# Kernel tuning notes

Hardware: AMD Instinct MI355X
Metric: run time of the kernel (lower is better)

## Reference

```python
import jax, jax.numpy as jnp
import numpy as np

B, TQ, TY = 8, 400, 400
Q_DIM, Y_DIM, ATT_DIM = 256, 256, 128


def setup_inputs() -> dict:
    key = jax.random.key(0)
    ks = jax.random.split(key, 9)
    s_q = 1.0 / np.sqrt(Q_DIM)
    s_y = 1.0 / np.sqrt(Y_DIM)
    s_a = 1.0 / np.sqrt(ATT_DIM)
    return {
        "query": jax.random.normal(ks[0], (B, TQ, Q_DIM), jnp.float32),
        "y": jax.random.normal(ks[1], (B, TY, Y_DIM), jnp.float32),
        "Wq_w": jax.random.uniform(ks[2], (ATT_DIM, Q_DIM), jnp.float32, -s_q, s_q),
        "Wq_b": jax.random.uniform(ks[3], (ATT_DIM,), jnp.float32, -s_q, s_q),
        "Wy_w": jax.random.uniform(ks[4], (ATT_DIM, Y_DIM), jnp.float32, -s_y, s_y),
        "Wy_b": jax.random.uniform(ks[5], (ATT_DIM,), jnp.float32, -s_y, s_y),
        "v_w": jax.random.uniform(ks[6], (1, ATT_DIM), jnp.float32, -s_a, s_a),
        "v_b": jax.random.uniform(ks[7], (1,), jnp.float32, -s_a, s_a),
        "n_wins_y": jax.random.randint(ks[8], (B,), TY // 2, TY + 1, jnp.int64 if jax.config.jax_enable_x64 else jnp.int32),
    }


def reference(query, y, Wq_w, Wq_b, Wy_w, Wy_b, v_w, v_b, n_wins_y):
    # Bahdanau scores: tanh(Wq(q)[:,None,:,:] + Wy(y)[:,:,None,:]) -> [B,Ty,Tq,A]
    q_proj = jnp.einsum('bqd,ad->bqa', query, Wq_w) + Wq_b      # [B,Tq,A]
    y_proj = jnp.einsum('btd,ad->bta', y, Wy_w) + Wy_b          # [B,Ty,A]
    h = jnp.tanh(q_proj[:, None, :, :] + y_proj[:, :, None, :])  # [B,Ty,Tq,A]
    att = jnp.einsum('btqa,a->btq', h, v_w[0]) + v_b[0]          # [B,Ty,Tq]
    att = jnp.transpose(att, (0, 2, 1))                          # [B,Tq,Ty]
    # mask invalid y windows (dim 2 = Ty), then softmax over Ty
    mask = jnp.arange(att.shape[2])[None, None, :] < n_wins_y[:, None, None]
    att = jnp.where(mask, att, -jnp.inf)
    att = jax.nn.softmax(att, axis=2)
    # soft attention apply: bmm(att, y) -> [B,Tq,y_dim]
    return jnp.einsum('bqt,btd->bqd', att, y)
```

## Files before the change

kernel.cpp:

```cpp
#include <hip/hip_runtime.h>


#define LOG2E 1.4426950408889634f
#define TANH_SCALE 2.8853900817779268f

constexpr int TQn = 400, TYn = 400, AD = 128, DD = 256;

__global__ __launch_bounds__(128) void transpose_kernel(
    const float* __restrict__ Wq, const float* __restrict__ Wy,
    const float* __restrict__ vw,
    float4* __restrict__ WTq, float4* __restrict__ WTy,
    float* __restrict__ vneg)
{
    const int k4 = blockIdx.x & 63;
    const bool isq = blockIdx.x < 64;
    const float4* src = reinterpret_cast<const float4*>(isq ? Wq : Wy);
    float4* dst = isq ? WTq : WTy;
    const int a = threadIdx.x;
    dst[k4 * 128 + a] = src[a * 64 + k4];
    if (blockIdx.x == 0) vneg[a] = -2.f * vw[a];
}

__global__ __launch_bounds__(256, 4) void proj_kernel(
    const float* __restrict__ qin, const float* __restrict__ yin,
    const float4* __restrict__ WTq, const float* __restrict__ bq,
    const float4* __restrict__ WTy, const float* __restrict__ by,
    float* __restrict__ EqS, float* __restrict__ EyT)
{
    const int blk = blockIdx.x;
    const bool is_q = blk < 800;
    const int row0 = (is_q ? blk : blk - 800) * 4;
    const float* in   = (is_q ? qin : yin) + (size_t)row0 * DD;
    const float4* wt  = is_q ? WTq : WTy;
    const float* bias = is_q ? bq : by;

    __shared__ float lin[4 * DD];
    __shared__ float red[4][AD];
    {
        const float4* in4 = reinterpret_cast<const float4*>(in);
        reinterpret_cast<float4*>(lin)[threadIdx.x] = in4[threadIdx.x];
    }
    __syncthreads();

    const int a = threadIdx.x & 127;
    const int h = threadIdx.x >> 7;
    float acc[4] = {0.f, 0.f, 0.f, 0.f};
    const float4* l4 = reinterpret_cast<const float4*>(lin);
    #pragma unroll 8
    for (int i = 0; i < 32; ++i) {
        const int k4 = h * 32 + i;
        float4 w4 = wt[k4 * 128 + a];
        #pragma unroll
        for (int r = 0; r < 4; ++r) {
            float4 v = l4[r * 64 + k4];
            acc[r] = fmaf(w4.x, v.x, acc[r]);
            acc[r] = fmaf(w4.y, v.y, acc[r]);
            acc[r] = fmaf(w4.z, v.z, acc[r]);
            acc[r] = fmaf(w4.w, v.w, acc[r]);
        }
    }
    if (h) {
        #pragma unroll
        for (int r = 0; r < 4; ++r) red[r][a] = acc[r];
    }
    __syncthreads();
    if (!h) {
        const float bb = bias[a];
        const int a4 = a >> 2, ac = a & 3;
        const int qoff = (row0 & 7);
        #pragma unroll
        for (int r = 0; r < 4; ++r) {
            const float e = __builtin_amdgcn_exp2f(
                (acc[r] + red[r][a] + bb) * TANH_SCALE);
            if (is_q)
                EqS[(size_t)(row0 >> 3) * 1024 + a4 * 32 + (qoff + r) * 4 + ac] = e;
            else
                EyT[(size_t)a4 * 12800 + (size_t)(row0 + r) * 4 + ac] = e;
        }
    }
}

__global__ __launch_bounds__(448, 2) void score_kernel(
    const float* __restrict__ EqS,
    const float4* __restrict__ EyT4,
    const float* __restrict__ vneg,
    const int*  __restrict__ nwins,
    float* __restrict__ s)
{
    const int grp = blockIdx.x;
    const int b   = grp / 100;
    const int qg  = grp % 100;
    const int q0  = qg * 4;
    const int n   = nwins[b];
    const int t   = threadIdx.x;
    if ((t & ~63) >= n) return;

    const int ycol = b * TYn + min(t, TYn - 1);
    const float4* eqg = reinterpret_cast<const float4*>(EqS)
                      + (size_t)(b * 50 + (qg >> 1)) * 256 + 4 * (qg & 1);
    const float4* vn4 = reinterpret_cast<const float4*>(vneg);

    float ac0 = 0.f, ac1 = 0.f, ac2 = 0.f, ac3 = 0.f;
    for (int a4 = 0; a4 < 32; ++a4) {
        const float4 ey = EyT4[(size_t)a4 * 3200 + ycol];
        const float4* eqa = eqg + a4 * 8;
        const float4 vv = vn4[a4];
        const float4 e0 = eqa[0], e1 = eqa[1], e2 = eqa[2], e3 = eqa[3];
        #define SCORE_Q(ACC, EQ)                                            \
        {                                                                   \
            float a0 = fmaf(EQ.x, ey.x, 1.f);                               \
            float a1 = fmaf(EQ.y, ey.y, 1.f);                               \
            float a2 = fmaf(EQ.z, ey.z, 1.f);                               \
            float a3 = fmaf(EQ.w, ey.w, 1.f);                               \
            float p01 = a0 * a1, p23 = a2 * a3;                             \
            float R = __builtin_amdgcn_rcpf(p01 * p23);                     \
            float u = p23 * R, w = p01 * R;                                 \
            ACC = fmaf(vv.x, a1 * u, ACC);                                  \
            ACC = fmaf(vv.y, a0 * u, ACC);                                  \
            ACC = fmaf(vv.z, a3 * w, ACC);                                  \
            ACC = fmaf(vv.w, a2 * w, ACC);                                  \
        }
        SCORE_Q(ac0, e0) SCORE_Q(ac1, e1) SCORE_Q(ac2, e2) SCORE_Q(ac3, e3)
        #undef SCORE_Q
    }
    if (t < n) {
        float* srow = s + (size_t)(b * TQn + q0) * TYn + t;
        srow[0 * TYn] = ac0; srow[1 * TYn] = ac1;
        srow[2 * TYn] = ac2; srow[3 * TYn] = ac3;
    }
}

__global__ __launch_bounds__(256, 4) void apply_kernel(
    const float* __restrict__ y,
    const float* __restrict__ s,
    const int*  __restrict__ nwins,
    float* __restrict__ out)
{
    const int bid = blockIdx.x;
    const int b   = bid / 100;
    const int q0  = (bid % 100) * 4;
    const int tid = threadIdx.x, wave = tid >> 6, lane = tid & 63;
    const int n = nwins[b];
    const float NEG_INF = -__builtin_inff();

    __shared__ float  s_p[4][408];
    __shared__ float4 s_y[2][16 * 64];

    const float4* yb = reinterpret_cast<const float4*>(y) + (size_t)(b * TYn) * 64;
    const int scol = tid & 63, srow0 = tid >> 6;
    float4 g0 = yb[(size_t)(srow0     ) * 64 + scol];
    float4 g1 = yb[(size_t)(srow0 +  4) * 64 + scol];
    float4 g2 = yb[(size_t)(srow0 +  8) * 64 + scol];
    float4 g3 = yb[(size_t)(srow0 + 12) * 64 + scol];

    const float* srow = s + (size_t)(b * TQn + q0 + wave) * TYn;
    float sc0, sc1, sc2, sc3, sc4, sc5, sc6;
    {
        int t;
        t = 0 * 64 + lane; sc0 = (t < n) ? srow[t] : NEG_INF;
        t = 1 * 64 + lane; sc1 = (t < n) ? srow[t] : NEG_INF;
        t = 2 * 64 + lane; sc2 = (t < n) ? srow[t] : NEG_INF;
        t = 3 * 64 + lane; sc3 = (t < n) ? srow[t] : NEG_INF;
        t = 4 * 64 + lane; sc4 = (t < n) ? srow[t] : NEG_INF;
        t = 5 * 64 + lane; sc5 = (t < n) ? srow[t] : NEG_INF;
        t = 6 * 64 + lane; sc6 = (t < n) ? srow[t] : NEG_INF;
    }
    float m = fmaxf(fmaxf(fmaxf(sc0, sc1), fmaxf(sc2, sc3)),
                    fmaxf(fmaxf(sc4, sc5), sc6));
    #pragma unroll
    for (int off = 32; off >= 1; off >>= 1) m = fmaxf(m, __shfl_xor(m, off, 64));
    sc0 = __builtin_amdgcn_exp2f((sc0 - m) * LOG2E);
    sc1 = __builtin_amdgcn_exp2f((sc1 - m) * LOG2E);
    sc2 = __builtin_amdgcn_exp2f((sc2 - m) * LOG2E);
    sc3 = __builtin_amdgcn_exp2f((sc3 - m) * LOG2E);
    sc4 = __builtin_amdgcn_exp2f((sc4 - m) * LOG2E);
    sc5 = __builtin_amdgcn_exp2f((sc5 - m) * LOG2E);
    sc6 = __builtin_amdgcn_exp2f((sc6 - m) * LOG2E);
    float l = ((sc0 + sc1) + (sc2 + sc3)) + ((sc4 + sc5) + sc6);
    #pragma unroll
    for (int off = 32; off >= 1; off >>= 1) l += __shfl_xor(l, off, 64);
    const float inv = 1.0f / l;
    s_p[wave][0 * 64 + lane] = sc0 * inv;
    s_p[wave][1 * 64 + lane] = sc1 * inv;
    s_p[wave][2 * 64 + lane] = sc2 * inv;
    s_p[wave][3 * 64 + lane] = sc3 * inv;
    s_p[wave][4 * 64 + lane] = sc4 * inv;
    s_p[wave][5 * 64 + lane] = sc5 * inv;
    {
        const int t = 6 * 64 + lane;
        if (t < TYn) s_p[wave][t] = sc6 * inv;
    }

    const int q  = lane >> 4;
    const int d4 = (wave << 4) | (lane & 15);
    float4 acc = {0.f, 0.f, 0.f, 0.f};
    const int ntile = (n + 15) >> 4;

    __syncthreads();
    for (int i = 0; i < ntile; ++i) {
        float4* buf = s_y[i & 1];
        buf[(srow0     ) * 64 + scol] = g0;
        buf[(srow0 +  4) * 64 + scol] = g1;
        buf[(srow0 +  8) * 64 + scol] = g2;
        buf[(srow0 + 12) * 64 + scol] = g3;
        if (i + 1 < ntile) {
            const int t0n = (i + 1) * 16;
            g0 = yb[(size_t)(t0n + srow0     ) * 64 + scol];
            g1 = yb[(size_t)(t0n + srow0 +  4) * 64 + scol];
            g2 = yb[(size_t)(t0n + srow0 +  8) * 64 + scol];
            g3 = yb[(size_t)(t0n + srow0 + 12) * 64 + scol];
        }
        __syncthreads();
        const int tb = i * 16;
        #pragma unroll
        for (int ttl = 0; ttl < 16; ++ttl) {
            const float  pt = s_p[q][tb + ttl];
            const float4 yv = buf[ttl * 64 + d4];
            acc.x = fmaf(pt, yv.x, acc.x);
            acc.y = fmaf(pt, yv.y, acc.y);
            acc.z = fmaf(pt, yv.z, acc.z);
            acc.w = fmaf(pt, yv.w, acc.w);
        }
    }
    reinterpret_cast<float4*>(out)[(size_t)(b * TQn + q0 + q) * 64 + d4] = acc;
}

extern "C" void kernel_launch(void* const* d_in, const int* in_sizes, int n_in,
                              void* d_out, int out_size, void* d_ws, size_t ws_size,
                              hipStream_t stream) {
    const float* query = (const float*)d_in[0];
    const float* y     = (const float*)d_in[1];
    const float* Wq_w  = (const float*)d_in[2];
    const float* Wq_b  = (const float*)d_in[3];
    const float* Wy_w  = (const float*)d_in[4];
    const float* Wy_b  = (const float*)d_in[5];
    const float* v_w   = (const float*)d_in[6];
    const int* nw      = (const int*)d_in[8];
    float* out = (float*)d_out;

    float4* WTq  = (float4*)d_ws;
    float4* WTy  = WTq + 64 * 128;
    float*  vneg = (float*)(WTy + 64 * 128);
    float*  EqS  = vneg + 256;
    float*  EyT  = EqS + (size_t)400 * 1024;
    float*  s    = EyT + (size_t)32 * 3200 * 4;

    transpose_kernel<<<128, 128, 0, stream>>>(Wq_w, Wy_w, v_w, WTq, WTy, vneg);
    proj_kernel<<<1600, 256, 0, stream>>>(query, y, WTq, Wq_b, WTy, Wy_b, EqS, EyT);
    score_kernel<<<8 * 100, 448, 0, stream>>>(
        EqS, (const float4*)EyT, vneg, nw, s);
    apply_kernel<<<8 * 100, 256, 0, stream>>>(y, s, nw, out);
}
```

Baseline: 64.98 us.

## Restructure apply kernel to stream y from global into registers, 8 queries per block

The apply kernel now handles 8 queries per block with 512 threads instead of 4 queries with 256. It drops the double-buffered LDS staging of y tiles and its per-tile barriers. Each thread loads its y slice straight from global memory into a register double buffer and reads probabilities from LDS as float4. The loop always covers all 400 positions, relying on zero probabilities for masked positions rather than stopping at n. This removes LDS traffic and synchronisation but halves the block count, depends on the cache for y reuse, and adds work on the masked tail.

Result: slower. 91.08 us (+40.2%).

```diff
diff --git a/kernel.cpp b/kernel.cpp
--- a/kernel.cpp
+++ b/kernel.cpp
@@ -5,6 +5,7 @@
 #define TANH_SCALE 2.8853900817779268f
 
 constexpr int TQn = 400, TYn = 400, AD = 128, DD = 256;
+constexpr int PROW = 404;
 
 __global__ __launch_bounds__(128) void transpose_kernel(
     const float* __restrict__ Wq, const float* __restrict__ Wy,
@@ -130,28 +131,20 @@
     }
 }
 
-__global__ __launch_bounds__(256, 4) void apply_kernel(
+__global__ __launch_bounds__(512, 2) void apply_kernel(
     const float* __restrict__ y,
     const float* __restrict__ s,
     const int*  __restrict__ nwins,
     float* __restrict__ out)
 {
     const int bid = blockIdx.x;
-    const int b   = bid / 100;
-    const int q0  = (bid % 100) * 4;
+    const int b   = bid / 50;
+    const int q0  = (bid % 50) * 8;
     const int tid = threadIdx.x, wave = tid >> 6, lane = tid & 63;
     const int n = nwins[b];
     const float NEG_INF = -__builtin_inff();
 
-    __shared__ float  s_p[4][408];
-    __shared__ float4 s_y[2][16 * 64];
-
-    const float4* yb = reinterpret_cast<const float4*>(y) + (size_t)(b * TYn) * 64;
-    const int scol = tid & 63, srow0 = tid >> 6;
-    float4 g0 = yb[(size_t)(srow0     ) * 64 + scol];
-    float4 g1 = yb[(size_t)(srow0 +  4) * 64 + scol];
-    float4 g2 = yb[(size_t)(srow0 +  8) * 64 + scol];
-    float4 g3 = yb[(size_t)(srow0 + 12) * 64 + scol];
+    __shared__ __align__(16) float s_p[8][PROW];
 
     const float* srow = s + (size_t)(b * TQn + q0 + wave) * TYn;
     float sc0, sc1, sc2, sc3, sc4, sc5, sc6;
@@ -190,36 +183,48 @@
         const int t = 6 * 64 + lane;
         if (t < TYn) s_p[wave][t] = sc6 * inv;
     }
-
-    const int q  = lane >> 4;
-    const int d4 = (wave << 4) | (lane & 15);
+    __syncthreads();
+
+    const int q  = lane >> 3;
+    const int d4 = (wave << 3) | (lane & 7);
+    const float4* prow4 = reinterpret_cast<const float4*>(&s_p[q][0]);
+    const float4* yb4 = reinterpret_cast<const float4*>(y) + (size_t)(b * TYn) * 64;
     float4 acc = {0.f, 0.f, 0.f, 0.f};
-    const int ntile = (n + 15) >> 4;
-
-    __syncthreads();
-    for (int i = 0; i < ntile; ++i) {
-        float4* buf = s_y[i & 1];
-        buf[(srow0     ) * 64 + scol] = g0;
-        buf[(srow0 +  4) * 64 + scol] = g1;
-        buf[(srow0 +  8) * 64 + scol] = g2;
-        buf[(srow0 + 12) * 64 + scol] = g3;
-        if (i + 1 < ntile) {
-            const int t0n = (i + 1) * 16;
-            g0 = yb[(size_t)(t0n + srow0     ) * 64 + scol];
-            g1 = yb[(size_t)(t0n + srow0 +  4) * 64 + scol];
-            g2 = yb[(size_t)(t0n + srow0 +  8) * 64 + scol];
-            g3 = yb[(size_t)(t0n + srow0 + 12) * 64 + scol];
-        }
-        __syncthreads();
-        const int tb = i * 16;
-        #pragma unroll
-        for (int ttl = 0; ttl < 16; ++ttl) {
-            const float  pt = s_p[q][tb + ttl];
-            const float4 yv = buf[ttl * 64 + d4];
-            acc.x = fmaf(pt, yv.x, acc.x);
-            acc.y = fmaf(pt, yv.y, acc.y);
-            acc.z = fmaf(pt, yv.z, acc.z);
-            acc.w = fmaf(pt, yv.w, acc.w);
+
+    float4 a0 = yb4[      d4], a1 = yb4[ 64 + d4], a2 = yb4[128 + d4], a3 = yb4[192 + d4];
+    float4 b0 = yb4[256 + d4], b1 = yb4[320 + d4], b2 = yb4[384 + d4], b3 = yb4[448 + d4];
+
+    #pragma unroll 2
+    for (int t4 = 0; t4 < 100; t4 += 2) {
+        {
+            const float4 pv = prow4[t4];
+            acc.x = fmaf(pv.x, a0.x, acc.x); acc.y = fmaf(pv.x, a0.y, acc.y);
+            acc.z = fmaf(pv.x, a0.z, acc.z); acc.w = fmaf(pv.x, a0.w, acc.w);
+            acc.x = fmaf(pv.y, a1.x, acc.x); acc.y = fmaf(pv.y, a1.y, acc.y);
+            acc.z = fmaf(pv.y, a1.z, acc.z); acc.w = fmaf(pv.y, a1.w, acc.w);
+            acc.x = fmaf(pv.z, a2.x, acc.x); acc.y = fmaf(pv.z, a2.y, acc.y);
+            acc.z = fmaf(pv.z, a2.z, acc.z); acc.w = fmaf(pv.z, a2.w, acc.w);
+            acc.x = fmaf(pv.w, a3.x, acc.x); acc.y = fmaf(pv.w, a3.y, acc.y);
+            acc.z = fmaf(pv.w, a3.z, acc.z); acc.w = fmaf(pv.w, a3.w, acc.w);
+            if (t4 + 2 < 100) {
+                const float4* yr = yb4 + (size_t)(t4 + 2) * 256;
+                a0 = yr[d4]; a1 = yr[64 + d4]; a2 = yr[128 + d4]; a3 = yr[192 + d4];
+            }
+        }
+        {
+            const float4 pv = prow4[t4 + 1];
+            acc.x = fmaf(pv.x, b0.x, acc.x); acc.y = fmaf(pv.x, b0.y, acc.y);
+            acc.z = fmaf(pv.x, b0.z, acc.z); acc.w = fmaf(pv.x, b0.w, acc.w);
+            acc.x = fmaf(pv.y, b1.x, acc.x); acc.y = fmaf(pv.y, b1.y, acc.y);
+            acc.z = fmaf(pv.y, b1.z, acc.z); acc.w = fmaf(pv.y, b1.w, acc.w);
+            acc.x = fmaf(pv.z, b2.x, acc.x); acc.y = fmaf(pv.z, b2.y, acc.y);
+            acc.z = fmaf(pv.z, b2.z, acc.z); acc.w = fmaf(pv.z, b2.w, acc.w);
+            acc.x = fmaf(pv.w, b3.x, acc.x); acc.y = fmaf(pv.w, b3.y, acc.y);
+            acc.z = fmaf(pv.w, b3.z, acc.z); acc.w = fmaf(pv.w, b3.w, acc.w);
+            if (t4 + 3 < 100) {
+                const float4* yr = yb4 + (size_t)(t4 + 3) * 256;
+                b0 = yr[d4]; b1 = yr[64 + d4]; b2 = yr[128 + d4]; b3 = yr[192 + d4];
+            }
         }
     }
     reinterpret_cast<float4*>(out)[(size_t)(b * TQn + q0 + q) * 64 + d4] = acc;
@@ -249,5 +254,5 @@
     proj_kernel<<<1600, 256, 0, stream>>>(query, y, WTq, Wq_b, WTy, Wy_b, EqS, EyT);
     score_kernel<<<8 * 100, 448, 0, stream>>>(
         EqS, (const float4*)EyT, vneg, nw, s);
-    apply_kernel<<<8 * 100, 256, 0, stream>>>(y, s, nw, out);
-}
+    apply_kernel<<<8 * 50, 512, 0, stream>>>(y, s, nw, out);
+}
```

## Fuse score, softmax and attention-apply into one kernel

Applied to the files above, without the earlier changes.

Merges the score kernel and the apply kernel into a single kernel. Each block computes the 4x400 score tile, runs a block-wide softmax through LDS reductions, and multiplies the probabilities with y, with waves splitting the Ty rows and a final cross-wave reduction in LDS. This removes the global round-trip of the score matrix and one kernel launch. It also rewrites the score inner math to use a single combined numerator per reciprocal. The cost is that early-exit waves are no longer skipped: all 448 threads run the score loop and the apply loop over every row regardless of n, and extra syncs and LDS reductions are added.

After: 61.67 us. 5.1% less time.

```diff
diff --git a/kernel.cpp b/kernel.cpp
--- a/kernel.cpp
+++ b/kernel.cpp
@@ -80,22 +80,28 @@
     }
 }
 
-__global__ __launch_bounds__(448, 2) void score_kernel(
+__global__ __launch_bounds__(448, 2) void fused_kernel(
     const float* __restrict__ EqS,
     const float4* __restrict__ EyT4,
     const float* __restrict__ vneg,
+    const float* __restrict__ y,
     const int*  __restrict__ nwins,
-    float* __restrict__ s)
+    float* __restrict__ out)
 {
     const int grp = blockIdx.x;
     const int b   = grp / 100;
     const int qg  = grp % 100;
     const int q0  = qg * 4;
     const int n   = nwins[b];
-    const int t   = threadIdx.x;
-    if ((t & ~63) >= n) return;
-
-    const int ycol = b * TYn + min(t, TYn - 1);
+    const int tid = threadIdx.x;
+    const int wave = tid >> 6, lane = tid & 63;
+    const float NEG_INF = -__builtin_inff();
+
+    __shared__ __align__(16) float4 s_pT[448];
+    __shared__ __align__(16) float4 s_rbuf[7 * 128];
+    __shared__ float s_wred[2][7][4];
+
+    const int ycol = b * TYn + min(tid, TYn - 1);
     const float4* eqg = reinterpret_cast<const float4*>(EqS)
                       + (size_t)(b * 50 + (qg >> 1)) * 256 + 4 * (qg & 1);
     const float4* vn4 = reinterpret_cast<const float4*>(vneg);
@@ -112,117 +118,136 @@
             float a1 = fmaf(EQ.y, ey.y, 1.f);                               \
             float a2 = fmaf(EQ.z, ey.z, 1.f);                               \
             float a3 = fmaf(EQ.w, ey.w, 1.f);                               \
-            float p01 = a0 * a1, p23 = a2 * a3;                             \
-            float R = __builtin_amdgcn_rcpf(p01 * p23);                     \
-            float u = p23 * R, w = p01 * R;                                 \
-            ACC = fmaf(vv.x, a1 * u, ACC);                                  \
-            ACC = fmaf(vv.y, a0 * u, ACC);                                  \
-            ACC = fmaf(vv.z, a3 * w, ACC);                                  \
-            ACC = fmaf(vv.w, a2 * w, ACC);                                  \
+            float n01 = fmaf(vv.x, a1, vv.y * a0);                          \
+            float n23 = fmaf(vv.z, a3, vv.w * a2);                          \
+            float d01 = a0 * a1, d23 = a2 * a3;                             \
+            float N = fmaf(n01, d23, n23 * d01);                            \
+            float R = __builtin_amdgcn_rcpf(d01 * d23);                     \
+            ACC = fmaf(N, R, ACC);                                          \
         }
         SCORE_Q(ac0, e0) SCORE_Q(ac1, e1) SCORE_Q(ac2, e2) SCORE_Q(ac3, e3)
         #undef SCORE_Q
     }
-    if (t < n) {
-        float* srow = s + (size_t)(b * TQn + q0) * TYn + t;
-        srow[0 * TYn] = ac0; srow[1 * TYn] = ac1;
-        srow[2 * TYn] = ac2; srow[3 * TYn] = ac3;
-    }
-}
-
-__global__ __launch_bounds__(256, 4) void apply_kernel(
-    const float* __restrict__ y,
-    const float* __restrict__ s,
-    const int*  __restrict__ nwins,
-    float* __restrict__ out)
-{
-    const int bid = blockIdx.x;
-    const int b   = bid / 100;
-    const int q0  = (bid % 100) * 4;
-    const int tid = threadIdx.x, wave = tid >> 6, lane = tid & 63;
-    const int n = nwins[b];
-    const float NEG_INF = -__builtin_inff();
-
-    __shared__ float  s_p[4][408];
-    __shared__ float4 s_y[2][16 * 64];
-
-    const float4* yb = reinterpret_cast<const float4*>(y) + (size_t)(b * TYn) * 64;
-    const int scol = tid & 63, srow0 = tid >> 6;
-    float4 g0 = yb[(size_t)(srow0     ) * 64 + scol];
-    float4 g1 = yb[(size_t)(srow0 +  4) * 64 + scol];
-    float4 g2 = yb[(size_t)(srow0 +  8) * 64 + scol];
-    float4 g3 = yb[(size_t)(srow0 + 12) * 64 + scol];
-
-    const float* srow = s + (size_t)(b * TQn + q0 + wave) * TYn;
-    float sc0, sc1, sc2, sc3, sc4, sc5, sc6;
-    {
-        int t;
-        t = 0 * 64 + lane; sc0 = (t < n) ? srow[t] : NEG_INF;
-        t = 1 * 64 + lane; sc1 = (t < n) ? srow[t] : NEG_INF;
-        t = 2 * 64 + lane; sc2 = (t < n) ? srow[t] : NEG_INF;
-        t = 3 * 64 + lane; sc3 = (t < n) ? srow[t] : NEG_INF;
-        t = 4 * 64 + lane; sc4 = (t < n) ? srow[t] : NEG_INF;
-        t = 5 * 64 + lane; sc5 = (t < n) ? srow[t] : NEG_INF;
-        t = 6 * 64 + lane; sc6 = (t < n) ? srow[t] : NEG_INF;
-    }
-    float m = fmaxf(fmaxf(fmaxf(sc0, sc1), fmaxf(sc2, sc3)),
-                    fmaxf(fmaxf(sc4, sc5), sc6));
-    #pragma unroll
-    for (int off = 32; off >= 1; off >>= 1) m = fmaxf(m, __shfl_xor(m, off, 64));
-    sc0 = __builtin_amdgcn_exp2f((sc0 - m) * LOG2E);
-    sc1 = __builtin_amdgcn_exp2f((sc1 - m) * LOG2E);
-    sc2 = __builtin_amdgcn_exp2f((sc2 - m) * LOG2E);
-    sc3 = __builtin_amdgcn_exp2f((sc3 - m) * LOG2E);
-    sc4 = __builtin_amdgcn_exp2f((sc4 - m) * LOG2E);
-    sc5 = __builtin_amdgcn_exp2f((sc5 - m) * LOG2E);
-    sc6 = __builtin_amdgcn_exp2f((sc6 - m) * LOG2E);
-    float l = ((sc0 + sc1) + (sc2 + sc3)) + ((sc4 + sc5) + sc6);
-    #pragma unroll
-    for (int off = 32; off >= 1; off >>= 1) l += __shfl_xor(l, off, 64);
-    const float inv = 1.0f / l;
-    s_p[wave][0 * 64 + lane] = sc0 * inv;
-    s_p[wave][1 * 64 + lane] = sc1 * inv;
-    s_p[wave][2 * 64 + lane] = sc2 * inv;
-    s_p[wave][3 * 64 + lane] = sc3 * inv;
-    s_p[wave][4 * 64 + lane] = sc4 * inv;
-    s_p[wave][5 * 64 + lane] = sc5 * inv;
-    {
-        const int t = 6 * 64 + lane;
-        if (t < TYn) s_p[wave][t] = sc6 * inv;
-    }
-
-    const int q  = lane >> 4;
-    const int d4 = (wave << 4) | (lane & 15);
-    float4 acc = {0.f, 0.f, 0.f, 0.f};
-    const int ntile = (n + 15) >> 4;
-
-    __syncthreads();
-    for (int i = 0; i < ntile; ++i) {
-        float4* buf = s_y[i & 1];
-        buf[(srow0     ) * 64 + scol] = g0;
-        buf[(srow0 +  4) * 64 + scol] = g1;
-        buf[(srow0 +  8) * 64 + scol] = g2;
-        buf[(srow0 + 12) * 64 + scol] = g3;
-        if (i + 1 < ntile) {
-            const int t0n = (i + 1) * 16;
-            g0 = yb[(size_t)(t0n + srow0     ) * 64 + scol];
-            g1 = yb[(size_t)(t0n + srow0 +  4) * 64 + scol];
-            g2 = yb[(size_t)(t0n + srow0 +  8) * 64 + scol];
-            g3 = yb[(size_t)(t0n + srow0 + 12) * 64 + scol];
-        }
+    if (tid >= n) { ac0 = NEG_INF; ac1 = NEG_INF; ac2 = NEG_INF; ac3 = NEG_INF; }
+
+    float m0 = ac0, m1 = ac1, m2 = ac2, m3 = ac3;
+    #pragma unroll
+    for (int off = 32; off >= 1; off >>= 1) {
+        m0 = fmaxf(m0, __shfl_xor(m0, off, 64));
+        m1 = fmaxf(m1, __shfl_xor(m1, off, 64));
+        m2 = fmaxf(m2, __shfl_xor(m2, off, 64));
+        m3 = fmaxf(m3, __shfl_xor(m3, off, 64));
+    }
+    if (lane == 0) {
+        s_wred[0][wave][0] = m0; s_wred[0][wave][1] = m1;
+        s_wred[0][wave][2] = m2; s_wred[0][wave][3] = m3;
+    }
+    __syncthreads();
+    m0 = s_wred[0][0][0]; m1 = s_wred[0][0][1];
+    m2 = s_wred[0][0][2]; m3 = s_wred[0][0][3];
+    #pragma unroll
+    for (int w2 = 1; w2 < 7; ++w2) {
+        m0 = fmaxf(m0, s_wred[0][w2][0]); m1 = fmaxf(m1, s_wred[0][w2][1]);
+        m2 = fmaxf(m2, s_wred[0][w2][2]); m3 = fmaxf(m3, s_wred[0][w2][3]);
+    }
+    float p0 = __builtin_amdgcn_exp2f((ac0 - m0) * LOG2E);
+    float p1 = __builtin_amdgcn_exp2f((ac1 - m1) * LOG2E);
+    float p2 = __builtin_amdgcn_exp2f((ac2 - m2) * LOG2E);
+    float p3 = __builtin_amdgcn_exp2f((ac3 - m3) * LOG2E);
+    float l0 = p0, l1 = p1, l2 = p2, l3 = p3;
+    #pragma unroll
+    for (int off = 32; off >= 1; off >>= 1) {
+        l0 += __shfl_xor(l0, off, 64);
+        l1 += __shfl_xor(l1, off, 64);
+        l2 += __shfl_xor(l2, off, 64);
+        l3 += __shfl_xor(l3, off, 64);
+    }
+    if (lane == 0) {
+        s_wred[1][wave][0] = l0; s_wred[1][wave][1] = l1;
+        s_wred[1][wave][2] = l2; s_wred[1][wave][3] = l3;
+    }
+    __syncthreads();
+    l0 = s_wred[1][0][0]; l1 = s_wred[1][0][1];
+    l2 = s_wred[1][0][2]; l3 = s_wred[1][0][3];
+    #pragma unroll
+    for (int w2 = 1; w2 < 7; ++w2) {
+        l0 += s_wred[1][w2][0]; l1 += s_wred[1][w2][1];
+        l2 += s_wred[1][w2][2]; l3 += s_wred[1][w2][3];
+    }
+    float4 pv;
+    pv.x = p0 * (1.0f / l0);
+    pv.y = p1 * (1.0f / l1);
+    pv.z = p2 * (1.0f / l2);
+    pv.w = p3 * (1.0f / l3);
+    s_pT[tid] = pv;
+    __syncthreads();
+
+    const float4* yb4 = reinterpret_cast<const float4*>(y) + (size_t)(b * TYn) * 64;
+    float4 A0 = {0,0,0,0}, A1 = {0,0,0,0}, A2 = {0,0,0,0}, A3 = {0,0,0,0};
+
+    int rA = wave;
+    float4 yA = yb4[(size_t)min(rA, TYn - 1) * 64 + lane];
+    float4 pA = s_pT[rA];
+    int rB = wave + 7;
+    float4 yB = yb4[(size_t)min(rB, TYn - 1) * 64 + lane];
+    float4 pB = s_pT[rB];
+
+    for (int i = 0; i < 29; ++i) {
+        {
+            const float4 yc = yA, pc = pA;
+            if (i < 28) {
+                const int rn = rA + 14;
+                yA = yb4[(size_t)min(rn, TYn - 1) * 64 + lane];
+                pA = s_pT[rn];
+                rA = rn;
+            }
+            A0.x = fmaf(pc.x, yc.x, A0.x); A0.y = fmaf(pc.x, yc.y, A0.y);
+            A0.z = fmaf(pc.x, yc.z, A0.z); A0.w = fmaf(pc.x, yc.w, A0.w);
+            A1.x = fmaf(pc.y, yc.x, A1.x); A1.y = fmaf(pc.y, yc.y, A1.y);
+            A1.z = fmaf(pc.y, yc.z, A1.z); A1.w = fmaf(pc.y, yc.w, A1.w);
+            A2.x = fmaf(pc.z, yc.x, A2.x); A2.y = fmaf(pc.z, yc.y, A2.y);
+            A2.z = fmaf(pc.z, yc.z, A2.z); A2.w = fmaf(pc.z, yc.w, A2.w);
+            A3.x = fmaf(pc.w, yc.x, A3.x); A3.y = fmaf(pc.w, yc.y, A3.y);
+            A3.z = fmaf(pc.w, yc.z, A3.z); A3.w = fmaf(pc.w, yc.w, A3.w);
+        }
+        {
+            const float4 yc = yB, pc = pB;
+            if (i < 28) {
+                const int rn = rB + 14;
+                yB = yb4[(size_t)min(rn, TYn - 1) * 64 + lane];
+                pB = s_pT[rn];
+                rB = rn;
+            }
+            A0.x = fmaf(pc.x, yc.x, A0.x); A0.y = fmaf(pc.x, yc.y, A0.y);
+            A0.z = fmaf(pc.x, yc.z, A0.z); A0.w = fmaf(pc.x, yc.w, A0.w);
+            A1.x = fmaf(pc.y, yc.x, A1.x); A1.y = fmaf(pc.y, yc.y, A1.y);
+            A1.z = fmaf(pc.y, yc.z, A1.z); A1.w = fmaf(pc.y, yc.w, A1.w);
+            A2.x = fmaf(pc.z, yc.x, A2.x); A2.y = fmaf(pc.z, yc.y, A2.y);
+            A2.z = fmaf(pc.z, yc.z, A2.z); A2.w = fmaf(pc.z, yc.w, A2.w);
+            A3.x = fmaf(pc.w, yc.x, A3.x); A3.y = fmaf(pc.w, yc.y, A3.y);
+            A3.z = fmaf(pc.w, yc.z, A3.z); A3.w = fmaf(pc.w, yc.w, A3.w);
+        }
+    }
+
+    float4* o4 = reinterpret_cast<float4*>(out) + (size_t)(b * TQn + q0) * 64;
+    auto rphase = [&](float4 AQ, float4 BQ, int PH) {
         __syncthreads();
-        const int tb = i * 16;
-        #pragma unroll
-        for (int ttl = 0; ttl < 16; ++ttl) {
-            const float  pt = s_p[q][tb + ttl];
-            const float4 yv = buf[ttl * 64 + d4];
-            acc.x = fmaf(pt, yv.x, acc.x);
-            acc.y = fmaf(pt, yv.y, acc.y);
-            acc.z = fmaf(pt, yv.z, acc.z);
-            acc.w = fmaf(pt, yv.w, acc.w);
-        }
-    }
-    reinterpret_cast<float4*>(out)[(size_t)(b * TQn + q0 + q) * 64 + d4] = acc;
+        s_rbuf[wave * 128 + lane]      = AQ;
+        s_rbuf[wave * 128 + 64 + lane] = BQ;
+        __syncthreads();
+        if (tid < 128) {
+            const int qi = tid >> 6, dr = tid & 63;
+            float4 s0 = s_rbuf[qi * 64 + dr];
+            #pragma unroll
+            for (int w2 = 1; w2 < 7; ++w2) {
+                float4 v = s_rbuf[w2 * 128 + qi * 64 + dr];
+                s0.x += v.x; s0.y += v.y; s0.z += v.z; s0.w += v.w;
+            }
+            o4[(size_t)(PH * 2 + qi) * 64 + dr] = s0;
+        }
+    };
+    rphase(A0, A1, 0);
+    rphase(A2, A3, 1);
 }
 
 extern "C" void kernel_launch(void* const* d_in, const int* in_sizes, int n_in,
@@ -243,11 +268,9 @@
     float*  vneg = (float*)(WTy + 64 * 128);
     float*  EqS  = vneg + 256;
     float*  EyT  = EqS + (size_t)400 * 1024;
-    float*  s    = EyT + (size_t)32 * 3200 * 4;
 
     transpose_kernel<<<128, 128, 0, stream>>>(Wq_w, Wy_w, v_w, WTq, WTy, vneg);
     proj_kernel<<<1600, 256, 0, stream>>>(query, y, WTq, Wq_b, WTy, Wy_b, EqS, EyT);
-    score_kernel<<<8 * 100, 448, 0, stream>>>(
-        EqS, (const float4*)EyT, vneg, nw, s);
-    apply_kernel<<<8 * 100, 256, 0, stream>>>(y, s, nw, out);
-}
+    fused_kernel<<<8 * 100, 448, 0, stream>>>(
+        EqS, (const float4*)EyT, vneg, y, nw, out);
+}
```
